# Optimization experiments

Measured on AMD Instinct MI355X. Metric: run time of the kernel, lower is better.

## Reference

```python
import jax, jax.numpy as jnp
import numpy as np

N = 50000     # nodes
E = 800000    # edges (avg degree 16)
DIN = 128     # in_size
DH = 256      # hidden_size
P = 100000    # pos/neg edge pairs


def _w(key, fan_in, shape):
    return jax.random.normal(key, shape, jnp.float32) * (1.0 / np.sqrt(fan_in))


def setup_inputs() -> dict:
    key = jax.random.key(0)
    ks = jax.random.split(key, 24)
    inp = {}
    inp['x'] = jax.random.normal(ks[0], (N, DIN), jnp.float32)
    inp['edge_src'] = jax.random.randint(ks[1], (E,), 0, N, dtype=jnp.int32)
    inp['edge_dst'] = jax.random.randint(ks[2], (E,), 0, N, dtype=jnp.int32)
    inp['pos_src'] = jax.random.randint(ks[3], (P,), 0, N, dtype=jnp.int32)
    inp['pos_dst'] = jax.random.randint(ks[4], (P,), 0, N, dtype=jnp.int32)
    inp['neg_src'] = jax.random.randint(ks[5], (P,), 0, N, dtype=jnp.int32)
    inp['neg_dst'] = jax.random.randint(ks[6], (P,), 0, N, dtype=jnp.int32)
    # SAGEConv layers: fc_self + fc_neigh + bias
    dims = [(DIN, DH), (DH, DH), (DH, DH)]
    for i, (di, do) in enumerate(dims):
        inp[f'Ws{i}'] = _w(ks[7 + 3 * i], di, (di, do))
        inp[f'Wn{i}'] = _w(ks[8 + 3 * i], di, (di, do))
        inp[f'b{i}'] = jnp.zeros((do,), jnp.float32)
    # predictor MLP: DH -> DH -> DH -> 1
    inp['Wp1'] = _w(ks[16], DH, (DH, DH)); inp['bp1'] = jnp.zeros((DH,), jnp.float32)
    inp['Wp2'] = _w(ks[17], DH, (DH, DH)); inp['bp2'] = jnp.zeros((DH,), jnp.float32)
    inp['Wp3'] = _w(ks[18], DH, (DH, 1)); inp['bp3'] = jnp.zeros((1,), jnp.float32)
    return inp


def _sage_layer(h, src, dst, Ws, Wn, b):
    # mean aggregation over incoming edges, then fc_self(h) + fc_neigh(agg) + b
    n = h.shape[0]
    msg = h[src]                                              # [E, d] gather
    deg = jax.ops.segment_sum(jnp.ones((src.shape[0],), h.dtype), dst, num_segments=n)
    agg = jax.ops.segment_sum(msg, dst, num_segments=n)
    agg = agg / jnp.maximum(deg, 1.0)[:, None]
    return h @ Ws + agg @ Wn + b


def reference(x, edge_src, edge_dst, pos_src, pos_dst, neg_src, neg_dst,
              Ws0, Wn0, b0, Ws1, Wn1, b1, Ws2, Wn2, b2,
              Wp1, bp1, Wp2, bp2, Wp3, bp3):
    h = x
    layers = [(Ws0, Wn0, b0), (Ws1, Wn1, b1), (Ws2, Wn2, b2)]
    for i, (Ws, Wn, bb) in enumerate(layers):
        h = _sage_layer(h, edge_src, edge_dst, Ws, Wn, bb)
        if i < len(layers) - 1:
            h = jax.nn.relu(h)

    def predictor(e):
        z = jax.nn.relu(e @ Wp1 + bp1)
        z = jax.nn.relu(z @ Wp2 + bp2)
        return z @ Wp3 + bp3

    hidden_pos = predictor(h[pos_src] * h[pos_dst])   # [P, 1]
    hidden_neg = predictor(h[neg_src] * h[neg_dst])   # [P, 1]
    return (hidden_pos, hidden_neg)
```

## Files before the change

### kernel.cpp

```cpp
#include <hip/hip_runtime.h>
#include <hip/hip_bf16.h>

#define CDIV(a, b) (((a) + (b) - 1) / (b))

typedef __attribute__((ext_vector_type(8))) __bf16 bf16x8;
typedef __attribute__((ext_vector_type(2))) __bf16 bf16x2;
typedef __attribute__((ext_vector_type(4))) float f32x4;

__device__ __forceinline__ float bf2f(unsigned short u) {
  union { unsigned int i; float f; } c; c.i = ((unsigned int)u) << 16; return c.f;
}
__device__ __forceinline__ unsigned short f2bf(float f) {
  union { float f; unsigned int i; } c; c.f = f;
  unsigned int r = c.i + 0x7fffu + ((c.i >> 16) & 1u);
  return (unsigned short)(r >> 16);
}
__device__ __forceinline__ unsigned int cvt2(float a, float b) {
  bf16x2 v; v[0] = (__bf16)a; v[1] = (__bf16)b;
  union { bf16x2 v; unsigned int u; } c; c.v = v; return c.u;
}
__device__ __forceinline__ unsigned short cvt1(float a) {
  __bf16 b = (__bf16)a;
  union { __bf16 b; unsigned short u; } c; c.b = b; return c.u;
}
__device__ __forceinline__ float dec1(unsigned int u) {
  union { unsigned int i; float f; } a, b;
  a.i = u << 16; b.i = u & 0xffff0000u;
  return a.f + b.f;
}
__device__ __forceinline__ unsigned int packhl(float v) {
  __bf16 h = (__bf16)v;
  float hf = (float)h;
  __bf16 l = (__bf16)(v - hf);
  bf16x2 p; p[0] = h; p[1] = l;
  union { bf16x2 v; unsigned int u; } c; c.v = p; return c.u;
}

__global__ void k_detect(const unsigned short* __restrict__ xq, int nsamp, int* __restrict__ flagp) {
  __shared__ float sm[256];
  int t = threadIdx.x;
  float mx = 0.f;
  for (int i = t; i < nsamp; i += 256) {
    float v = bf2f(xq[i]);
    if (!(v == v)) v = 1e30f;
    mx = fmaxf(mx, fabsf(v));
  }
  sm[t] = mx; __syncthreads();
  for (int o = 128; o > 0; o >>= 1) {
    if (t < o) sm[t] = fmaxf(sm[t], sm[t + o]);
    __syncthreads();
  }
  if (t == 0) *flagp = (sm[0] > 1e6f) ? 1 : 0;
}

__global__ void k_cvt7(const void* p0, const void* p1, const void* p2, const void* p3,
                       const void* p4, const void* p5, const void* p6,
                       float* d0, float* d1, float* d2, float* d3,
                       float* d4, float* d5, float* d6, const int* __restrict__ flagp) {
  int b = blockIdx.x, t = threadIdx.x;
  const void* s = 0; float* d = 0; int n = 256;
  switch (b) {
    case 0: s = p0; d = d0; break;
    case 1: s = p1; d = d1; break;
    case 2: s = p2; d = d2; break;
    case 3: s = p3; d = d3; break;
    case 4: s = p4; d = d4; break;
    case 5: s = p5; d = d5; break;
    default: s = p6; d = d6; n = 1; break;
  }
  if (t < n) d[t] = (*flagp) ? ((const float*)s)[t] : bf2f(((const unsigned short*)s)[t]);
}

__global__ void k_wh(const void* __restrict__ W, unsigned short* __restrict__ Bth,
                     int K, const int* __restrict__ flagp) {
  int i = blockIdx.x * 256 + threadIdx.x;
  if (i >= K * 256) return;
  int k = i >> 8, n = i & 255;
  float v = (*flagp) ? ((const float*)W)[i] : bf2f(((const unsigned short*)W)[i]);
  Bth[(size_t)n * K + k] = f2bf(v);
}

__global__ void k_xbf16(const void* __restrict__ x, unsigned short* __restrict__ Xb, int n,
                        const int* __restrict__ flagp) {
  int i = blockIdx.x * 256 + threadIdx.x;
  if (i >= n) return;
  float v = (*flagp) ? ((const float*)x)[i] : bf2f(((const unsigned short*)x)[i]);
  Xb[i] = f2bf(v);
}

__global__ void k_zero_i32(int* p, int n) {
  int i = blockIdx.x * 256 + threadIdx.x;
  if (i < n) p[i] = 0;
}

__global__ void k_deg(const int* __restrict__ dst, int* __restrict__ deg, int E) {
  int e = blockIdx.x * 256 + threadIdx.x;
  if (e < E) atomicAdd(&deg[dst[e]], 1);
}
__global__ void k_scan1(const int* __restrict__ in, int* __restrict__ out, int* __restrict__ bsums, int n) {
  __shared__ int sh[256];
  int t = threadIdx.x, i = blockIdx.x * 256 + t;
  int v = (i < n) ? in[i] : 0;
  sh[t] = v; __syncthreads();
  for (int o = 1; o < 256; o <<= 1) {
    int add = (t >= o) ? sh[t - o] : 0;
    __syncthreads();
    sh[t] += add;
    __syncthreads();
  }
  if (i < n) out[i] = sh[t] - v;
  if (t == 255) bsums[blockIdx.x] = sh[255];
}
__global__ void k_scan2(int* bsums, int nb) {
  __shared__ int sh[256];
  int t = threadIdx.x;
  int v = (t < nb) ? bsums[t] : 0;
  sh[t] = v; __syncthreads();
  for (int o = 1; o < 256; o <<= 1) {
    int add = (t >= o) ? sh[t - o] : 0;
    __syncthreads();
    sh[t] += add;
    __syncthreads();
  }
  if (t < nb) bsums[t] = sh[t] - v;
}
__global__ void k_scan3(int* offs, const int* bsums, int n, int etot) {
  int i = blockIdx.x * 256 + threadIdx.x;
  if (i < n) offs[i] += bsums[blockIdx.x];
  if (i == 0) offs[n] = etot;
}
__global__ void k_copy_i32(const int* __restrict__ a, int* __restrict__ b, int n) {
  int i = blockIdx.x * 256 + threadIdx.x;
  if (i < n) b[i] = a[i];
}
__global__ void k_fill(const int* __restrict__ dst, const int* __restrict__ src,
                       int* __restrict__ cursor, int* __restrict__ csr_src, int E) {
  int e = blockIdx.x * 256 + threadIdx.x;
  if (e >= E) return;
  int pos = atomicAdd(&cursor[dst[e]], 1);
  csr_src[pos] = src[e];
}
__global__ void k_sortw(const int* __restrict__ offs, int* __restrict__ csr, int n) {
  int w = threadIdx.x >> 6, lane = threadIdx.x & 63;
  int v = blockIdx.x * 4 + w;
  if (v >= n) return;
  int s = offs[v], e = offs[v + 1];
  int deg = e - s;
  if (deg <= 1) return;
  if (deg > 64) {
    if (lane == 0) {
      for (int i = s + 1; i < e; ++i) {
        int key = csr[i], j = i - 1;
        while (j >= s && csr[j] > key) { csr[j + 1] = csr[j]; --j; }
        csr[j + 1] = key;
      }
    }
    return;
  }
  int val = (lane < deg) ? csr[s + lane] : 0x7fffffff;
#pragma unroll
  for (int k = 2; k <= 64; k <<= 1) {
    bool dir = (lane & k) == 0;
#pragma unroll
    for (int j = k >> 1; j > 0; j >>= 1) {
      int p = __shfl_xor(val, j, 64);
      bool lower = (lane & j) == 0;
      val = (lower == dir) ? min(val, p) : max(val, p);
    }
  }
  if (lane < deg) csr[s + lane] = val;
}

__global__ void k_aggfuse(const unsigned int* __restrict__ Yp, const unsigned short* __restrict__ Zh,
                          const int* __restrict__ offs, const int* __restrict__ csr,
                          const float* __restrict__ bias, int relu,
                          unsigned short* __restrict__ Hb) {
  int w = threadIdx.x >> 6, lane = threadIdx.x & 63;
  int v = blockIdx.x * 4 + w;
  int c4 = lane * 4;
  uint4 yq = *(const uint4*)&Yp[(size_t)v * 256 + c4];
  int s = offs[v], e = offs[v + 1];
  float a0 = 0.f, a1 = 0.f, a2 = 0.f, a3 = 0.f;
  int i = s;
  for (; i + 2 <= e; i += 2) {
    uint2 z0 = *(const uint2*)&Zh[(size_t)csr[i] * 256 + c4];
    uint2 z1 = *(const uint2*)&Zh[(size_t)csr[i + 1] * 256 + c4];
    a0 += bf2f((unsigned short)z0.x) + bf2f((unsigned short)z1.x);
    a1 += bf2f((unsigned short)(z0.x >> 16)) + bf2f((unsigned short)(z1.x >> 16));
    a2 += bf2f((unsigned short)z0.y) + bf2f((unsigned short)z1.y);
    a3 += bf2f((unsigned short)(z0.y >> 16)) + bf2f((unsigned short)(z1.y >> 16));
  }
  if (i < e) {
    uint2 z0 = *(const uint2*)&Zh[(size_t)csr[i] * 256 + c4];
    a0 += bf2f((unsigned short)z0.x);
    a1 += bf2f((unsigned short)(z0.x >> 16));
    a2 += bf2f((unsigned short)z0.y);
    a3 += bf2f((unsigned short)(z0.y >> 16));
  }
  float inv = 1.f / fmaxf((float)(e - s), 1.f);
  float4 bv = *(const float4*)&bias[c4];
  float r0 = dec1(yq.x) + a0 * inv + bv.x;
  float r1 = dec1(yq.y) + a1 * inv + bv.y;
  float r2 = dec1(yq.z) + a2 * inv + bv.z;
  float r3 = dec1(yq.w) + a3 * inv + bv.w;
  if (relu) {
    r0 = fmaxf(r0, 0.f); r1 = fmaxf(r1, 0.f);
    r2 = fmaxf(r2, 0.f); r3 = fmaxf(r3, 0.f);
  }
  uint2 o;
  o.x = cvt2(r0, r1);
  o.y = cvt2(r2, r3);
  *(uint2*)&Hb[(size_t)v * 256 + c4] = o;
}

__global__ __launch_bounds__(256) void gemm2(
    const unsigned short* __restrict__ Ab, int K,
    const unsigned short* __restrict__ B1h, const unsigned short* __restrict__ B2h,
    int M, unsigned int* __restrict__ O1p, unsigned short* __restrict__ O2b) {
  __shared__ unsigned short sAh[128 * 40], sBh[128 * 40];
  int t = threadIdx.x;
  int mt = blockIdx.x >> 2, nt = blockIdx.x & 3;
  int m0 = mt * 128;
  const unsigned short* Bh = (nt < 2) ? B1h : B2h;
  int n0 = (nt & 1) * 128;
  int wid = t >> 6, lane = t & 63;
  int wr = (wid >> 1) * 64, wc = (wid & 1) * 64;
  int quad = lane >> 4, lrow = lane & 15;

  f32x4 acc[4][4];
  const f32x4 z4 = {0.f, 0.f, 0.f, 0.f};
#pragma unroll
  for (int i = 0; i < 4; ++i)
#pragma unroll
    for (int j = 0; j < 4; ++j) acc[i][j] = z4;

  int sr = t >> 2;
  int c8 = (t & 3) * 8;

  for (int k0 = 0; k0 < K; k0 += 32) {
#pragma unroll
    for (int rep = 0; rep < 2; ++rep) {
      int r = sr + rep * 64;
      int arow = m0 + r; if (arow >= M) arow = M - 1;
      *(uint4*)&sAh[r * 40 + c8] = *(const uint4*)&Ab[(size_t)arow * K + k0 + c8];
      *(uint4*)&sBh[r * 40 + c8] = *(const uint4*)&Bh[(size_t)(n0 + r) * K + k0 + c8];
    }
    __syncthreads();
    bf16x8 ah[4], bh[4];
#pragma unroll
    for (int i = 0; i < 4; ++i) {
      ah[i] = *(const bf16x8*)&sAh[(wr + i * 16 + lrow) * 40 + quad * 8];
      bh[i] = *(const bf16x8*)&sBh[(wc + i * 16 + lrow) * 40 + quad * 8];
    }
#pragma unroll
    for (int i = 0; i < 4; ++i)
#pragma unroll
      for (int j = 0; j < 4; ++j)
        acc[i][j] = __builtin_amdgcn_mfma_f32_16x16x32_bf16(ah[i], bh[j], acc[i][j], 0, 0, 0);
    __syncthreads();
  }

#pragma unroll
  for (int j = 0; j < 4; ++j) {
    int gc = n0 + wc + j * 16 + lrow;
#pragma unroll
    for (int i = 0; i < 4; ++i) {
#pragma unroll
      for (int rr = 0; rr < 4; ++rr) {
        int gr = m0 + wr + i * 16 + quad * 4 + rr;
        if (gr < M) {
          float v = acc[i][j][rr];
          size_t idx = (size_t)gr * 256 + gc;
          if (nt < 2) O1p[idx] = packhl(v);
          else        O2b[idx] = cvt1(v);
        }
      }
    }
  }
}

__global__ __launch_bounds__(256, 3) void gemm_pred_fused(
    const unsigned short* __restrict__ Hb,
    const int* __restrict__ ps, const int* __restrict__ pd,
    const int* __restrict__ ns, const int* __restrict__ nd,
    int nPos,
    const unsigned short* __restrict__ B1h, const float* __restrict__ bp1c,
    const unsigned short* __restrict__ B2h, const float* __restrict__ bp2c,
    const float* __restrict__ wp3, const float* __restrict__ bp3c,
    void* __restrict__ out, const int* __restrict__ flagp) {
  __shared__ __align__(16) unsigned short zT[64 * 264];
  __shared__ __align__(16) unsigned short sBh[256 * 40];
  int t = threadIdx.x;
  int m0 = blockIdx.x * 64;
  int wid = t >> 6, lane = t & 63;
  int wc = wid * 64;
  int quad = lane >> 4, lrow = lane & 15;

  int sr = t >> 2;
  int c8 = (t & 3) * 8;
  int c64 = (t & 3) * 64;

  int arow = m0 + sr;
  int s, d;
  if (arow < nPos) { s = ps[arow]; d = pd[arow]; }
  else             { s = ns[arow - nPos]; d = nd[arow - nPos]; }
  const unsigned short* Hs = &Hb[(size_t)s * 256];
  const unsigned short* Hd = &Hb[(size_t)d * 256];

#pragma unroll
  for (int u = 0; u < 8; ++u) {
    uint4 hs = *(const uint4*)(Hs + c64 + u * 8);
    uint4 hd = *(const uint4*)(Hd + c64 + u * 8);
    uint4 o;
    o.x = cvt2(bf2f((unsigned short)hs.x) * bf2f((unsigned short)hd.x),
               bf2f((unsigned short)(hs.x >> 16)) * bf2f((unsigned short)(hd.x >> 16)));
    o.y = cvt2(bf2f((unsigned short)hs.y) * bf2f((unsigned short)hd.y),
               bf2f((unsigned short)(hs.y >> 16)) * bf2f((unsigned short)(hd.y >> 16)));
    o.z = cvt2(bf2f((unsigned short)hs.z) * bf2f((unsigned short)hd.z),
               bf2f((unsigned short)(hs.z >> 16)) * bf2f((unsigned short)(hd.z >> 16)));
    o.w = cvt2(bf2f((unsigned short)hs.w) * bf2f((unsigned short)hd.w),
               bf2f((unsigned short)(hs.w >> 16)) * bf2f((unsigned short)(hd.w >> 16)));
    *(uint4*)&zT[sr * 264 + c64 + u * 8] = o;
  }

  f32x4 acc[4][4];
  const f32x4 z4 = {0.f, 0.f, 0.f, 0.f};
#pragma unroll
  for (int i = 0; i < 4; ++i)
#pragma unroll
    for (int j = 0; j < 4; ++j) acc[i][j] = z4;

  for (int k0 = 0; k0 < 256; k0 += 32) {
#pragma unroll
    for (int rep = 0; rep < 4; ++rep) {
      int r = sr + rep * 64;
      *(uint4*)&sBh[r * 40 + c8] = *(const uint4*)&B1h[(size_t)r * 256 + k0 + c8];
    }
    __syncthreads();
    bf16x8 ah[4], bh[4];
#pragma unroll
    for (int i = 0; i < 4; ++i) {
      ah[i] = *(const bf16x8*)&zT[(i * 16 + lrow) * 264 + k0 + quad * 8];
      bh[i] = *(const bf16x8*)&sBh[(wc + i * 16 + lrow) * 40 + quad * 8];
    }
#pragma unroll
    for (int i = 0; i < 4; ++i)
#pragma unroll
      for (int j = 0; j < 4; ++j)
        acc[i][j] = __builtin_amdgcn_mfma_f32_16x16x32_bf16(ah[i], bh[j], acc[i][j], 0, 0, 0);
    __syncthreads();
  }

#pragma unroll
  for (int j = 0; j < 4; ++j) {
    int gc = wc + j * 16 + lrow;
    float bv = bp1c[gc];
#pragma unroll
    for (int i = 0; i < 4; ++i) {
#pragma unroll
      for (int rr = 0; rr < 4; ++rr) {
        int rloc = i * 16 + quad * 4 + rr;
        float v = fmaxf(acc[i][j][rr] + bv, 0.f);
        zT[rloc * 264 + gc] = cvt1(v);
      }
    }
  }

#pragma unroll
  for (int i = 0; i < 4; ++i)
#pragma unroll
    for (int j = 0; j < 4; ++j) acc[i][j] = z4;

  for (int k0 = 0; k0 < 256; k0 += 32) {
#pragma unroll
    for (int rep = 0; rep < 4; ++rep) {
      int r = sr + rep * 64;
      *(uint4*)&sBh[r * 40 + c8] = *(const uint4*)&B2h[(size_t)r * 256 + k0 + c8];
    }
    __syncthreads();
    bf16x8 ah[4], bh[4];
#pragma unroll
    for (int i = 0; i < 4; ++i) {
      ah[i] = *(const bf16x8*)&zT[(i * 16 + lrow) * 264 + k0 + quad * 8];
      bh[i] = *(const bf16x8*)&sBh[(wc + i * 16 + lrow) * 40 + quad * 8];
    }
#pragma unroll
    for (int i = 0; i < 4; ++i)
#pragma unroll
      for (int j = 0; j < 4; ++j)
        acc[i][j] = __builtin_amdgcn_mfma_f32_16x16x32_bf16(ah[i], bh[j], acc[i][j], 0, 0, 0);
    __syncthreads();
  }

  float* part = (float*)sBh;
  int cid = wid * 16 + lrow;
#pragma unroll
  for (int i = 0; i < 4; ++i) {
#pragma unroll
    for (int rr = 0; rr < 4; ++rr) {
      int rloc = i * 16 + quad * 4 + rr;
      float sum = 0.f;
#pragma unroll
      for (int j = 0; j < 4; ++j) {
        int gc = wc + j * 16 + lrow;
        float v = fmaxf(acc[i][j][rr] + bp2c[gc], 0.f);
        sum += v * wp3[gc];
      }
      part[rloc * 65 + cid] = sum;
    }
  }
  __syncthreads();
  if (t < 64) {
    int gr = m0 + t;
    float ssum = 0.f;
#pragma unroll
    for (int c = 0; c < 64; ++c) ssum += part[t * 65 + c];
    ssum += bp3c[0];
    if (*flagp) ((float*)out)[gr] = ssum;
    else        ((unsigned short*)out)[gr] = f2bf(ssum);
  }
}

extern "C" void kernel_launch(void* const* d_in, const int* in_sizes, int n_in,
                              void* d_out, int out_size, void* d_ws, size_t ws_size,
                              hipStream_t stream) {
  const int N = 50000, E = 800000, P = 100000, DIN = 128, DH = 256;
  const int M2 = 2 * P;
  const void* x = d_in[0];
  const int* esrc = (const int*)d_in[1];
  const int* edst = (const int*)d_in[2];
  const int* psrc = (const int*)d_in[3];
  const int* pdst = (const int*)d_in[4];
  const int* nsrc = (const int*)d_in[5];
  const int* ndst = (const int*)d_in[6];
  const void* Ws0 = d_in[7];  const void* Wn0 = d_in[8];  const void* b0 = d_in[9];
  const void* Ws1 = d_in[10]; const void* Wn1 = d_in[11]; const void* b1 = d_in[12];
  const void* Ws2 = d_in[13]; const void* Wn2 = d_in[14]; const void* b2 = d_in[15];
  const void* Wp1 = d_in[16]; const void* bp1 = d_in[17];
  const void* Wp2 = d_in[18]; const void* bp2 = d_in[19];
  const void* Wp3 = d_in[20]; const void* bp3 = d_in[21];
  (void)in_sizes; (void)n_in; (void)out_size; (void)ws_size;

  const size_t NH = (size_t)N * DH;
  unsigned short* Hb = (unsigned short*)d_ws;
  unsigned short* Xb = Hb;
  char* reg1 = (char*)d_ws + NH * 2;
  unsigned int* Yp = (unsigned int*)reg1;
  unsigned short* Zh = (unsigned short*)(reg1 + NH * 4);
  float* P0 = (float*)(reg1 + (size_t)M2 * 256 * 2);
  float* P1 = P0 + M2;
  unsigned short* W16 = (unsigned short*)(P1 + M2);
  unsigned short* ws0h = W16;
  unsigned short* wn0h = ws0h + 32768;
  unsigned short* ws1h = wn0h + 32768;
  unsigned short* wn1h = ws1h + 65536;
  unsigned short* ws2h = wn1h + 65536;
  unsigned short* wn2h = ws2h + 65536;
  unsigned short* wp1h = wn2h + 65536;
  unsigned short* wp2h = wp1h + 65536;
  float* FB = (float*)(wp2h + 65536);
  float* b0f  = FB;
  float* b1f  = b0f + 256;
  float* b2f  = b1f + 256;
  float* bp1f = b2f + 256;
  float* bp2f = bp1f + 256;
  float* wp3f = bp2f + 256;
  float* bp3f = wp3f + 256;
  int* deg   = (int*)(bp3f + 4);
  int* offs  = deg + N;
  int* cur   = offs + (N + 1);
  int* bsums = cur + N;
  int* csr   = bsums + 256;
  int* flagp = csr + E;

  k_detect<<<1, 256, 0, stream>>>((const unsigned short*)x, 8192, flagp);

  k_wh<<<CDIV(DIN * DH, 256), 256, 0, stream>>>(Ws0, ws0h, DIN, flagp);
  k_wh<<<CDIV(DIN * DH, 256), 256, 0, stream>>>(Wn0, wn0h, DIN, flagp);
  k_wh<<<CDIV(DH * DH, 256), 256, 0, stream>>>(Ws1, ws1h, DH, flagp);
  k_wh<<<CDIV(DH * DH, 256), 256, 0, stream>>>(Wn1, wn1h, DH, flagp);
  k_wh<<<CDIV(DH * DH, 256), 256, 0, stream>>>(Ws2, ws2h, DH, flagp);
  k_wh<<<CDIV(DH * DH, 256), 256, 0, stream>>>(Wn2, wn2h, DH, flagp);
  k_wh<<<CDIV(DH * DH, 256), 256, 0, stream>>>(Wp1, wp1h, DH, flagp);
  k_wh<<<CDIV(DH * DH, 256), 256, 0, stream>>>(Wp2, wp2h, DH, flagp);
  k_cvt7<<<7, 256, 0, stream>>>(b0, b1, b2, bp1, bp2, Wp3, bp3,
                                b0f, b1f, b2f, bp1f, bp2f, wp3f, bp3f, flagp);

  int nb = CDIV(N, 256);
  k_zero_i32<<<nb, 256, 0, stream>>>(deg, N);
  k_deg<<<CDIV(E, 256), 256, 0, stream>>>(edst, deg, E);
  k_scan1<<<nb, 256, 0, stream>>>(deg, offs, bsums, N);
  k_scan2<<<1, 256, 0, stream>>>(bsums, nb);
  k_scan3<<<nb, 256, 0, stream>>>(offs, bsums, N, E);
  k_copy_i32<<<nb, 256, 0, stream>>>(offs, cur, N);
  k_fill<<<CDIV(E, 256), 256, 0, stream>>>(edst, esrc, cur, csr, E);
  k_sortw<<<CDIV(N, 4), 256, 0, stream>>>(offs, csr, N);

  const int MT = CDIV(N, 128);

  k_xbf16<<<CDIV(N * DIN, 256), 256, 0, stream>>>(x, Xb, N * DIN, flagp);
  gemm2<<<MT * 4, 256, 0, stream>>>(Xb, DIN, ws0h, wn0h, N, Yp, Zh);
  k_aggfuse<<<N / 4, 256, 0, stream>>>(Yp, Zh, offs, csr, b0f, 1, Hb);

  gemm2<<<MT * 4, 256, 0, stream>>>(Hb, DH, ws1h, wn1h, N, Yp, Zh);
  k_aggfuse<<<N / 4, 256, 0, stream>>>(Yp, Zh, offs, csr, b1f, 1, Hb);

  gemm2<<<MT * 4, 256, 0, stream>>>(Hb, DH, ws2h, wn2h, N, Yp, Zh);
  k_aggfuse<<<N / 4, 256, 0, stream>>>(Yp, Zh, offs, csr, b2f, 0, Hb);

  gemm_pred_fused<<<M2 / 64, 256, 0, stream>>>(Hb, psrc, pdst, nsrc, ndst, P,
                                               wp1h, bp1f, wp2h, bp2f, wp3f, bp3f,
                                               d_out, flagp);
}
```

Measured before the change: 694.0 us.

## Hold predictor weight tiles in registers and swizzle the LDS activation tile

Result: slower. 721.5 us (+4.0%).

```diff
diff --git a/kernel.cpp b/kernel.cpp
--- a/kernel.cpp
+++ b/kernel.cpp
@@ -279,7 +279,7 @@
   }
 }
 
-__global__ __launch_bounds__(256, 3) void gemm_pred_fused(
+__global__ __launch_bounds__(256, 2) void gemm_pred_fused(
     const unsigned short* __restrict__ Hb,
     const int* __restrict__ ps, const int* __restrict__ pd,
     const int* __restrict__ ns, const int* __restrict__ nd,
@@ -289,7 +289,6 @@
     const float* __restrict__ wp3, const float* __restrict__ bp3c,
     void* __restrict__ out, const int* __restrict__ flagp) {
   __shared__ __align__(16) unsigned short zT[64 * 264];
-  __shared__ __align__(16) unsigned short sBh[256 * 40];
   int t = threadIdx.x;
   int m0 = blockIdx.x * 64;
   int wid = t >> 6, lane = t & 63;
@@ -297,20 +296,35 @@
   int quad = lane >> 4, lrow = lane & 15;
 
   int sr = t >> 2;
-  int c8 = (t & 3) * 8;
-  int c64 = (t & 3) * 64;
+  int cq = t & 3;
 
   int arow = m0 + sr;
   int s, d;
   if (arow < nPos) { s = ps[arow]; d = pd[arow]; }
   else             { s = ns[arow - nPos]; d = nd[arow - nPos]; }
-  const unsigned short* Hs = &Hb[(size_t)s * 256];
-  const unsigned short* Hd = &Hb[(size_t)d * 256];
-
+  const unsigned short* Hs = &Hb[(size_t)s * 256 + cq * 64];
+  const unsigned short* Hd = &Hb[(size_t)d * 256 + cq * 64];
+
+  uint4 ghs[8], ghd[8];
 #pragma unroll
   for (int u = 0; u < 8; ++u) {
-    uint4 hs = *(const uint4*)(Hs + c64 + u * 8);
-    uint4 hd = *(const uint4*)(Hd + c64 + u * 8);
+    ghs[u] = *(const uint4*)(Hs + u * 8);
+    ghd[u] = *(const uint4*)(Hd + u * 8);
+  }
+
+  bf16x8 breg[32];
+  {
+    const unsigned short* Bp = &B1h[(size_t)(wc + lrow) * 256 + quad * 8];
+#pragma unroll
+    for (int ss = 0; ss < 8; ++ss)
+#pragma unroll
+      for (int j = 0; j < 4; ++j)
+        breg[ss * 4 + j] = *(const bf16x8*)(Bp + j * 16 * 256 + ss * 32);
+  }
+
+#pragma unroll
+  for (int u = 0; u < 8; ++u) {
+    uint4 hs = ghs[u], hd = ghd[u];
     uint4 o;
     o.x = cvt2(bf2f((unsigned short)hs.x) * bf2f((unsigned short)hd.x),
                bf2f((unsigned short)(hs.x >> 16)) * bf2f((unsigned short)(hd.x >> 16)));
@@ -320,7 +334,7 @@
                bf2f((unsigned short)(hs.z >> 16)) * bf2f((unsigned short)(hd.z >> 16)));
     o.w = cvt2(bf2f((unsigned short)hs.w) * bf2f((unsigned short)hd.w),
                bf2f((unsigned short)(hs.w >> 16)) * bf2f((unsigned short)(hd.w >> 16)));
-    *(uint4*)&zT[sr * 264 + c64 + u * 8] = o;
+    *(uint4*)&zT[sr * 264 + cq * 64 + 8 * (u ^ cq)] = o;
   }
 
   f32x4 acc[4][4];
@@ -330,38 +344,47 @@
 #pragma unroll
     for (int j = 0; j < 4; ++j) acc[i][j] = z4;
 
-  for (int k0 = 0; k0 < 256; k0 += 32) {
-#pragma unroll
-    for (int rep = 0; rep < 4; ++rep) {
-      int r = sr + rep * 64;
-      *(uint4*)&sBh[r * 40 + c8] = *(const uint4*)&B1h[(size_t)r * 256 + k0 + c8];
-    }
-    __syncthreads();
-    bf16x8 ah[4], bh[4];
-#pragma unroll
-    for (int i = 0; i < 4; ++i) {
-      ah[i] = *(const bf16x8*)&zT[(i * 16 + lrow) * 264 + k0 + quad * 8];
-      bh[i] = *(const bf16x8*)&sBh[(wc + i * 16 + lrow) * 40 + quad * 8];
-    }
+  __syncthreads();
+
+#pragma unroll
+  for (int ss = 0; ss < 8; ++ss) {
+    bf16x8 ah[4];
 #pragma unroll
     for (int i = 0; i < 4; ++i)
+      ah[i] = *(const bf16x8*)&zT[(i * 16 + lrow) * 264 + ss * 32 + 8 * (quad ^ (ss >> 1))];
+#pragma unroll
+    for (int i = 0; i < 4; ++i)
 #pragma unroll
       for (int j = 0; j < 4; ++j)
-        acc[i][j] = __builtin_amdgcn_mfma_f32_16x16x32_bf16(ah[i], bh[j], acc[i][j], 0, 0, 0);
-    __syncthreads();
-  }
+        acc[i][j] = __builtin_amdgcn_mfma_f32_16x16x32_bf16(ah[i], breg[ss * 4 + j], acc[i][j], 0, 0, 0);
+  }
+
+  {
+    const unsigned short* Bp = &B2h[(size_t)(wc + lrow) * 256 + quad * 8];
+#pragma unroll
+    for (int ss = 0; ss < 8; ++ss)
+#pragma unroll
+      for (int j = 0; j < 4; ++j)
+        breg[ss * 4 + j] = *(const bf16x8*)(Bp + j * 16 * 256 + ss * 32);
+  }
+
+  __syncthreads();
 
 #pragma unroll
   for (int j = 0; j < 4; ++j) {
-    int gc = wc + j * 16 + lrow;
-    float bv = bp1c[gc];
+    int col = wc + j * 16 + lrow;
+    float bv = bp1c[col];
 #pragma unroll
     for (int i = 0; i < 4; ++i) {
 #pragma unroll
       for (int rr = 0; rr < 4; ++rr) {
         int rloc = i * 16 + quad * 4 + rr;
         float v = fmaxf(acc[i][j][rr] + bv, 0.f);
-        zT[rloc * 264 + gc] = cvt1(v);
+        float vn = __shfl_xor(v, 1, 64);
+        if (!(lrow & 1)) {
+          int c2 = col ^ (wid << 3);
+          *(unsigned int*)&zT[rloc * 264 + c2] = cvt2(v, vn);
+        }
       }
     }
   }
@@ -371,28 +394,24 @@
 #pragma unroll
     for (int j = 0; j < 4; ++j) acc[i][j] = z4;
 
-  for (int k0 = 0; k0 < 256; k0 += 32) {
-#pragma unroll
-    for (int rep = 0; rep < 4; ++rep) {
-      int r = sr + rep * 64;
-      *(uint4*)&sBh[r * 40 + c8] = *(const uint4*)&B2h[(size_t)r * 256 + k0 + c8];
-    }
-    __syncthreads();
-    bf16x8 ah[4], bh[4];
-#pragma unroll
-    for (int i = 0; i < 4; ++i) {
-      ah[i] = *(const bf16x8*)&zT[(i * 16 + lrow) * 264 + k0 + quad * 8];
-      bh[i] = *(const bf16x8*)&sBh[(wc + i * 16 + lrow) * 40 + quad * 8];
-    }
+  __syncthreads();
+
+#pragma unroll
+  for (int ss = 0; ss < 8; ++ss) {
+    bf16x8 ah[4];
 #pragma unroll
     for (int i = 0; i < 4; ++i)
+      ah[i] = *(const bf16x8*)&zT[(i * 16 + lrow) * 264 + ss * 32 + 8 * (quad ^ (ss >> 1))];
+#pragma unroll
+    for (int i = 0; i < 4; ++i)
 #pragma unroll
       for (int j = 0; j < 4; ++j)
-        acc[i][j] = __builtin_amdgcn_mfma_f32_16x16x32_bf16(ah[i], bh[j], acc[i][j], 0, 0, 0);
-    __syncthreads();
-  }
-
-  float* part = (float*)sBh;
+        acc[i][j] = __builtin_amdgcn_mfma_f32_16x16x32_bf16(ah[i], breg[ss * 4 + j], acc[i][j], 0, 0, 0);
+  }
+
+  __syncthreads();
+
+  float* part = (float*)zT;
   int cid = wid * 16 + lrow;
 #pragma unroll
   for (int i = 0; i < 4; ++i) {
@@ -406,7 +425,7 @@
         float v = fmaxf(acc[i][j][rr] + bp2c[gc], 0.f);
         sum += v * wp3[gc];
       }
-      part[rloc * 65 + cid] = sum;
+      part[rloc * 66 + cid] = sum;
     }
   }
   __syncthreads();
@@ -414,7 +433,7 @@
     int gr = m0 + t;
     float ssum = 0.f;
 #pragma unroll
-    for (int c = 0; c < 64; ++c) ssum += part[t * 65 + c];
+    for (int c = 0; c < 64; ++c) ssum += part[t * 66 + c];
     ssum += bp3c[0];
     if (*flagp) ((float*)out)[gr] = ssum;
     else        ((unsigned short*)out)[gr] = f2bf(ssum);
```

## Aggregate before transform and fuse self/neighbor GEMMs into one concat GEMM

Applied to the files above, without the earlier changes.

Measured after the change: 650.1 us. 6.3% less time.

```diff
diff --git a/kernel.cpp b/kernel.cpp
--- a/kernel.cpp
+++ b/kernel.cpp
@@ -22,18 +22,6 @@
 __device__ __forceinline__ unsigned short cvt1(float a) {
   __bf16 b = (__bf16)a;
   union { __bf16 b; unsigned short u; } c; c.b = b; return c.u;
-}
-__device__ __forceinline__ float dec1(unsigned int u) {
-  union { unsigned int i; float f; } a, b;
-  a.i = u << 16; b.i = u & 0xffff0000u;
-  return a.f + b.f;
-}
-__device__ __forceinline__ unsigned int packhl(float v) {
-  __bf16 h = (__bf16)v;
-  float hf = (float)h;
-  __bf16 l = (__bf16)(v - hf);
-  bf16x2 p; p[0] = h; p[1] = l;
-  union { bf16x2 v; unsigned int u; } c; c.v = p; return c.u;
 }
 
 __global__ void k_detect(const unsigned short* __restrict__ xq, int nsamp, int* __restrict__ flagp) {
@@ -171,58 +159,74 @@
   if (lane < deg) csr[s + lane] = val;
 }
 
-__global__ void k_aggfuse(const unsigned int* __restrict__ Yp, const unsigned short* __restrict__ Zh,
-                          const int* __restrict__ offs, const int* __restrict__ csr,
-                          const float* __restrict__ bias, int relu,
-                          unsigned short* __restrict__ Hb) {
+__global__ void k_agg(const unsigned short* __restrict__ H, int Kd,
+                      const int* __restrict__ offs, const int* __restrict__ csr,
+                      unsigned short* __restrict__ Ab) {
   int w = threadIdx.x >> 6, lane = threadIdx.x & 63;
   int v = blockIdx.x * 4 + w;
-  int c4 = lane * 4;
-  uint4 yq = *(const uint4*)&Yp[(size_t)v * 256 + c4];
   int s = offs[v], e = offs[v + 1];
-  float a0 = 0.f, a1 = 0.f, a2 = 0.f, a3 = 0.f;
-  int i = s;
-  for (; i + 2 <= e; i += 2) {
-    uint2 z0 = *(const uint2*)&Zh[(size_t)csr[i] * 256 + c4];
-    uint2 z1 = *(const uint2*)&Zh[(size_t)csr[i + 1] * 256 + c4];
-    a0 += bf2f((unsigned short)z0.x) + bf2f((unsigned short)z1.x);
-    a1 += bf2f((unsigned short)(z0.x >> 16)) + bf2f((unsigned short)(z1.x >> 16));
-    a2 += bf2f((unsigned short)z0.y) + bf2f((unsigned short)z1.y);
-    a3 += bf2f((unsigned short)(z0.y >> 16)) + bf2f((unsigned short)(z1.y >> 16));
-  }
-  if (i < e) {
-    uint2 z0 = *(const uint2*)&Zh[(size_t)csr[i] * 256 + c4];
-    a0 += bf2f((unsigned short)z0.x);
-    a1 += bf2f((unsigned short)(z0.x >> 16));
-    a2 += bf2f((unsigned short)z0.y);
-    a3 += bf2f((unsigned short)(z0.y >> 16));
-  }
   float inv = 1.f / fmaxf((float)(e - s), 1.f);
-  float4 bv = *(const float4*)&bias[c4];
-  float r0 = dec1(yq.x) + a0 * inv + bv.x;
-  float r1 = dec1(yq.y) + a1 * inv + bv.y;
-  float r2 = dec1(yq.z) + a2 * inv + bv.z;
-  float r3 = dec1(yq.w) + a3 * inv + bv.w;
-  if (relu) {
-    r0 = fmaxf(r0, 0.f); r1 = fmaxf(r1, 0.f);
-    r2 = fmaxf(r2, 0.f); r3 = fmaxf(r3, 0.f);
-  }
-  uint2 o;
-  o.x = cvt2(r0, r1);
-  o.y = cvt2(r2, r3);
-  *(uint2*)&Hb[(size_t)v * 256 + c4] = o;
-}
-
-__global__ __launch_bounds__(256) void gemm2(
-    const unsigned short* __restrict__ Ab, int K,
+  if (Kd == 256) {
+    int c4 = lane * 4;
+    float a0 = 0.f, a1 = 0.f, a2 = 0.f, a3 = 0.f;
+    int i = s;
+    for (; i + 4 <= e; i += 4) {
+      uint2 z0 = *(const uint2*)&H[(size_t)csr[i] * 256 + c4];
+      uint2 z1 = *(const uint2*)&H[(size_t)csr[i + 1] * 256 + c4];
+      uint2 z2 = *(const uint2*)&H[(size_t)csr[i + 2] * 256 + c4];
+      uint2 z3 = *(const uint2*)&H[(size_t)csr[i + 3] * 256 + c4];
+      a0 += bf2f((unsigned short)z0.x) + bf2f((unsigned short)z1.x)
+          + bf2f((unsigned short)z2.x) + bf2f((unsigned short)z3.x);
+      a1 += bf2f((unsigned short)(z0.x >> 16)) + bf2f((unsigned short)(z1.x >> 16))
+          + bf2f((unsigned short)(z2.x >> 16)) + bf2f((unsigned short)(z3.x >> 16));
+      a2 += bf2f((unsigned short)z0.y) + bf2f((unsigned short)z1.y)
+          + bf2f((unsigned short)z2.y) + bf2f((unsigned short)z3.y);
+      a3 += bf2f((unsigned short)(z0.y >> 16)) + bf2f((unsigned short)(z1.y >> 16))
+          + bf2f((unsigned short)(z2.y >> 16)) + bf2f((unsigned short)(z3.y >> 16));
+    }
+    for (; i < e; ++i) {
+      uint2 z0 = *(const uint2*)&H[(size_t)csr[i] * 256 + c4];
+      a0 += bf2f((unsigned short)z0.x);
+      a1 += bf2f((unsigned short)(z0.x >> 16));
+      a2 += bf2f((unsigned short)z0.y);
+      a3 += bf2f((unsigned short)(z0.y >> 16));
+    }
+    uint2 o;
+    o.x = cvt2(a0 * inv, a1 * inv);
+    o.y = cvt2(a2 * inv, a3 * inv);
+    *(uint2*)&Ab[(size_t)v * 256 + c4] = o;
+  } else {
+    int c2 = lane * 2;
+    float a0 = 0.f, a1 = 0.f;
+    int i = s;
+    for (; i + 4 <= e; i += 4) {
+      unsigned int z0 = *(const unsigned int*)&H[(size_t)csr[i] * 128 + c2];
+      unsigned int z1 = *(const unsigned int*)&H[(size_t)csr[i + 1] * 128 + c2];
+      unsigned int z2 = *(const unsigned int*)&H[(size_t)csr[i + 2] * 128 + c2];
+      unsigned int z3 = *(const unsigned int*)&H[(size_t)csr[i + 3] * 128 + c2];
+      a0 += bf2f((unsigned short)z0) + bf2f((unsigned short)z1)
+          + bf2f((unsigned short)z2) + bf2f((unsigned short)z3);
+      a1 += bf2f((unsigned short)(z0 >> 16)) + bf2f((unsigned short)(z1 >> 16))
+          + bf2f((unsigned short)(z2 >> 16)) + bf2f((unsigned short)(z3 >> 16));
+    }
+    for (; i < e; ++i) {
+      unsigned int z0 = *(const unsigned int*)&H[(size_t)csr[i] * 128 + c2];
+      a0 += bf2f((unsigned short)z0);
+      a1 += bf2f((unsigned short)(z0 >> 16));
+    }
+    *(unsigned int*)&Ab[(size_t)v * 128 + c2] = cvt2(a0 * inv, a1 * inv);
+  }
+}
+
+__global__ __launch_bounds__(256) void gemm_cat(
+    const unsigned short* __restrict__ A1, const unsigned short* __restrict__ A2, int K,
     const unsigned short* __restrict__ B1h, const unsigned short* __restrict__ B2h,
-    int M, unsigned int* __restrict__ O1p, unsigned short* __restrict__ O2b) {
+    const float* __restrict__ bias, int relu, int M, unsigned short* __restrict__ O) {
   __shared__ unsigned short sAh[128 * 40], sBh[128 * 40];
   int t = threadIdx.x;
-  int mt = blockIdx.x >> 2, nt = blockIdx.x & 3;
+  int mt = blockIdx.x >> 1, nt = blockIdx.x & 1;
   int m0 = mt * 128;
-  const unsigned short* Bh = (nt < 2) ? B1h : B2h;
-  int n0 = (nt & 1) * 128;
+  int n0 = nt * 128;
   int wid = t >> 6, lane = t & 63;
   int wr = (wid >> 1) * 64, wc = (wid & 1) * 64;
   int quad = lane >> 4, lrow = lane & 15;
@@ -237,42 +241,47 @@
   int sr = t >> 2;
   int c8 = (t & 3) * 8;
 
-  for (int k0 = 0; k0 < K; k0 += 32) {
-#pragma unroll
-    for (int rep = 0; rep < 2; ++rep) {
-      int r = sr + rep * 64;
-      int arow = m0 + r; if (arow >= M) arow = M - 1;
-      *(uint4*)&sAh[r * 40 + c8] = *(const uint4*)&Ab[(size_t)arow * K + k0 + c8];
-      *(uint4*)&sBh[r * 40 + c8] = *(const uint4*)&Bh[(size_t)(n0 + r) * K + k0 + c8];
-    }
-    __syncthreads();
-    bf16x8 ah[4], bh[4];
-#pragma unroll
-    for (int i = 0; i < 4; ++i) {
-      ah[i] = *(const bf16x8*)&sAh[(wr + i * 16 + lrow) * 40 + quad * 8];
-      bh[i] = *(const bf16x8*)&sBh[(wc + i * 16 + lrow) * 40 + quad * 8];
-    }
-#pragma unroll
-    for (int i = 0; i < 4; ++i)
-#pragma unroll
-      for (int j = 0; j < 4; ++j)
-        acc[i][j] = __builtin_amdgcn_mfma_f32_16x16x32_bf16(ah[i], bh[j], acc[i][j], 0, 0, 0);
-    __syncthreads();
+#pragma unroll
+  for (int pl = 0; pl < 2; ++pl) {
+    const unsigned short* Ap = pl ? A2 : A1;
+    const unsigned short* Bp = pl ? B2h : B1h;
+    for (int k0 = 0; k0 < K; k0 += 32) {
+#pragma unroll
+      for (int rep = 0; rep < 2; ++rep) {
+        int r = sr + rep * 64;
+        int arow = m0 + r; if (arow >= M) arow = M - 1;
+        *(uint4*)&sAh[r * 40 + c8] = *(const uint4*)&Ap[(size_t)arow * K + k0 + c8];
+        *(uint4*)&sBh[r * 40 + c8] = *(const uint4*)&Bp[(size_t)(n0 + r) * K + k0 + c8];
+      }
+      __syncthreads();
+      bf16x8 ah[4], bh[4];
+#pragma unroll
+      for (int i = 0; i < 4; ++i) {
+        ah[i] = *(const bf16x8*)&sAh[(wr + i * 16 + lrow) * 40 + quad * 8];
+        bh[i] = *(const bf16x8*)&sBh[(wc + i * 16 + lrow) * 40 + quad * 8];
+      }
+#pragma unroll
+      for (int i = 0; i < 4; ++i)
+#pragma unroll
+        for (int j = 0; j < 4; ++j)
+          acc[i][j] = __builtin_amdgcn_mfma_f32_16x16x32_bf16(ah[i], bh[j], acc[i][j], 0, 0, 0);
+      __syncthreads();
+    }
   }
 
 #pragma unroll
   for (int j = 0; j < 4; ++j) {
     int gc = n0 + wc + j * 16 + lrow;
+    float bv = bias[gc];
 #pragma unroll
     for (int i = 0; i < 4; ++i) {
 #pragma unroll
       for (int rr = 0; rr < 4; ++rr) {
         int gr = m0 + wr + i * 16 + quad * 4 + rr;
         if (gr < M) {
-          float v = acc[i][j][rr];
-          size_t idx = (size_t)gr * 256 + gc;
-          if (nt < 2) O1p[idx] = packhl(v);
-          else        O2b[idx] = cvt1(v);
+          float v = acc[i][j][rr] + bv;
+          if (relu) v = fmaxf(v, 0.f);
+          O[(size_t)gr * 256 + gc] = cvt1(v);
         }
       }
     }
@@ -442,11 +451,11 @@
   (void)in_sizes; (void)n_in; (void)out_size; (void)ws_size;
 
   const size_t NH = (size_t)N * DH;
-  unsigned short* Hb = (unsigned short*)d_ws;
-  unsigned short* Xb = Hb;
+  unsigned short* planeA = (unsigned short*)d_ws;
+  unsigned short* Xb = planeA;
   char* reg1 = (char*)d_ws + NH * 2;
-  unsigned int* Yp = (unsigned int*)reg1;
-  unsigned short* Zh = (unsigned short*)(reg1 + NH * 4);
+  unsigned short* AggB  = (unsigned short*)reg1;
+  unsigned short* planeB = (unsigned short*)(reg1 + NH * 4);
   float* P0 = (float*)(reg1 + (size_t)M2 * 256 * 2);
   float* P1 = P0 + M2;
   unsigned short* W16 = (unsigned short*)(P1 + M2);
@@ -496,19 +505,19 @@
   k_fill<<<CDIV(E, 256), 256, 0, stream>>>(edst, esrc, cur, csr, E);
   k_sortw<<<CDIV(N, 4), 256, 0, stream>>>(offs, csr, N);
 
-  const int MT = CDIV(N, 128);
+  const int G_L = CDIV(N, 128) * 2;
 
   k_xbf16<<<CDIV(N * DIN, 256), 256, 0, stream>>>(x, Xb, N * DIN, flagp);
-  gemm2<<<MT * 4, 256, 0, stream>>>(Xb, DIN, ws0h, wn0h, N, Yp, Zh);
-  k_aggfuse<<<N / 4, 256, 0, stream>>>(Yp, Zh, offs, csr, b0f, 1, Hb);
-
-  gemm2<<<MT * 4, 256, 0, stream>>>(Hb, DH, ws1h, wn1h, N, Yp, Zh);
-  k_aggfuse<<<N / 4, 256, 0, stream>>>(Yp, Zh, offs, csr, b1f, 1, Hb);
-
-  gemm2<<<MT * 4, 256, 0, stream>>>(Hb, DH, ws2h, wn2h, N, Yp, Zh);
-  k_aggfuse<<<N / 4, 256, 0, stream>>>(Yp, Zh, offs, csr, b2f, 0, Hb);
-
-  gemm_pred_fused<<<M2 / 64, 256, 0, stream>>>(Hb, psrc, pdst, nsrc, ndst, P,
+  k_agg<<<N / 4, 256, 0, stream>>>(Xb, DIN, offs, csr, AggB);
+  gemm_cat<<<G_L, 256, 0, stream>>>(Xb, AggB, DIN, ws0h, wn0h, b0f, 1, N, planeB);
+
+  k_agg<<<N / 4, 256, 0, stream>>>(planeB, DH, offs, csr, AggB);
+  gemm_cat<<<G_L, 256, 0, stream>>>(planeB, AggB, DH, ws1h, wn1h, b1f, 1, N, planeA);
+
+  k_agg<<<N / 4, 256, 0, stream>>>(planeA, DH, offs, csr, AggB);
+  gemm_cat<<<G_L, 256, 0, stream>>>(planeA, AggB, DH, ws2h, wn2h, b2f, 0, N, planeB);
+
+  gemm_pred_fused<<<M2 / 64, 256, 0, stream>>>(planeB, psrc, pdst, nsrc, ndst, P,
                                                wp1h, bp1f, wp2h, bp2f, wp3f, bp3f,
                                                d_out, flagp);
 }
```
